# Kernel optimization log

Hardware: AMD Instinct MI355X
Metric: run time of the kernel (lower is better)

## Reference

```python
import jax, jax.numpy as jnp
import numpy as np

MOMENTUM = 0.1  # matches init_kwargs


def _amp_norm(x, running_amp, momentum):
    # x: [B, C, H, W] real; running_amp: [C, H, W]
    fft = jnp.fft.fft2(x, axes=(-2, -1))            # [B,C,H,W] complex64
    amp = jnp.abs(fft)                               # amplitude spectrum
    pha = jnp.angle(fft)                             # phase spectrum
    amp_mean = amp.mean(axis=0)                      # batch-averaged amplitude [C,H,W]
    # First call (buffer all-zero): adopt batch amplitude; otherwise EMA update.
    new_amp = jnp.where(jnp.sum(running_amp) == 0,
                        amp_mean,
                        (1.0 - momentum) * running_amp + momentum * amp_mean)
    # Rebuild spectrum with shared (running) amplitude and per-sample phase.
    fft_new = new_amp[None].astype(jnp.complex64) * jnp.exp(1j * pha)
    x_out = jnp.real(jnp.fft.ifft2(fft_new, axes=(-2, -1))).astype(x.dtype)
    return x_out, new_amp


def setup_inputs() -> dict:
    key = jax.random.key(0)
    x = jax.random.normal(key, (32, 3, 384, 384), dtype=jnp.float32)
    running_amp = jnp.zeros((3, 384, 384), dtype=jnp.float32)
    return {"x": x, "running_amp": running_amp}


def reference(x, running_amp):
    x_out, _ = _amp_norm(x, running_amp, MOMENTUM)
    return x_out
```

## Files before the change

### kernel.cpp

```cpp
#include <hip/hip_runtime.h>
#include <math.h>


#define NFFT   384
#define NL     8
#define LSTR   385
#define PADW   200
#define PLANE  147456
#define IMGS   96

__device__ __forceinline__ float2 cmul(float2 a, float2 b) {
    return make_float2(a.x*b.x - a.y*b.y, a.x*b.y + a.y*b.x);
}

__device__ __forceinline__ void fill_tw(float2* tw) {
    for (int k = threadIdx.x; k < NFFT; k += 256) {
        float ang = (-6.28318530717958647692f / (float)NFFT) * (float)k;
        float sv, cv;
        sincosf(ang, &sv, &cv);
        tw[k] = make_float2(cv, sv);
    }
}

template<int DIR>
__device__ float2* fft_lines(float2* buf0, float2* buf1, const float2* tw) {
    const int line = threadIdx.x >> 5;
    const int lane = threadIdx.x & 31;
    const float dir = (float)DIR;
    float2* src = buf0;
    float2* dst = buf1;

    {
        float2* s = src + line * LSTR;
        float2* d = dst + line * LSTR;
        const float b3 = (DIR > 0) ? -0.86602540378443864676f : 0.86602540378443864676f;
        #pragma unroll
        for (int i = 0; i < 4; ++i) {
            int j = lane + 32 * i;
            float2 c0 = s[j], c1 = s[j + 128], c2 = s[j + 256];
            float2 t0 = make_float2(c1.x + c2.x, c1.y + c2.y);
            float2 dd = make_float2(c1.x - c2.x, c1.y - c2.y);
            float2 y0 = make_float2(c0.x + t0.x, c0.y + t0.y);
            float2 u1 = make_float2(c0.x - 0.5f * t0.x, c0.y - 0.5f * t0.y);
            float2 iv = make_float2(-b3 * dd.y, b3 * dd.x);
            float2 y1 = make_float2(u1.x + iv.x, u1.y + iv.y);
            float2 y2 = make_float2(u1.x - iv.x, u1.y - iv.y);
            float2 w1 = tw[j];      w1.y *= dir;
            float2 w2 = tw[2 * j];  w2.y *= dir;
            d[3 * j]     = y0;
            d[3 * j + 1] = cmul(w1, y1);
            d[3 * j + 2] = cmul(w2, y2);
        }
    }
    __syncthreads();
    { float2* t = src; src = dst; dst = t; }

    #pragma unroll
    for (int st = 0; st < 3; ++st) {
        const int m = 3 << (2 * st);
        float2* s = src + line * LSTR;
        float2* d = dst + line * LSTR;
        #pragma unroll
        for (int i = 0; i < 3; ++i) {
            int q  = lane + 32 * i;
            int k  = q % m;
            int jm = q - k;
            float2 a = s[q], b = s[q + 96], c = s[q + 192], e = s[q + 288];
            float2 acp = make_float2(a.x + c.x, a.y + c.y);
            float2 acm = make_float2(a.x - c.x, a.y - c.y);
            float2 bdp = make_float2(b.x + e.x, b.y + e.y);
            float2 bdm = make_float2(b.x - e.x, b.y - e.y);
            float2 ibd = make_float2(-dir * bdm.y, dir * bdm.x);
            float2 y0 = make_float2(acp.x + bdp.x, acp.y + bdp.y);
            float2 y2 = make_float2(acp.x - bdp.x, acp.y - bdp.y);
            float2 y1 = make_float2(acm.x - ibd.x, acm.y - ibd.y);
            float2 y3 = make_float2(acm.x + ibd.x, acm.y + ibd.y);
            float2 w1 = tw[jm];      w1.y *= dir;
            float2 w2 = tw[2 * jm];  w2.y *= dir;
            float2 w3 = tw[3 * jm];  w3.y *= dir;
            d[4 * jm + k]         = y0;
            d[4 * jm + k + m]     = cmul(w1, y1);
            d[4 * jm + k + 2 * m] = cmul(w2, y2);
            d[4 * jm + k + 3 * m] = cmul(w3, y3);
        }
        __syncthreads();
        float2* t = src; src = dst; dst = t;
    }

    {
        float2* s = src + line * LSTR;
        float2* d = dst + line * LSTR;
        #pragma unroll
        for (int i = 0; i < 6; ++i) {
            int q = lane + 32 * i;
            float2 a = s[q];
            float2 b = s[q + 192];
            d[q]       = make_float2(a.x + b.x, a.y + b.y);
            d[q + 192] = make_float2(a.x - b.x, a.y - b.y);
        }
        __syncthreads();
        float2* t = src; src = dst; dst = t;
    }
    return src;
}

__global__ __launch_bounds__(256) void k_fft_rows_fwd(const float* __restrict__ x,
                                                      float2* __restrict__ A) {
    __shared__ float2 tw[NFFT];
    __shared__ float2 b0[NL * LSTR];
    __shared__ float2 b1[NL * LSTR];
    int bx  = blockIdx.x;
    int img = bx / 24;
    int rg  = bx - img * 24;
    fill_tw(tw);
    int line = threadIdx.x >> 5, lane = threadIdx.x & 31;
    int pr   = rg * NL + line;
    const float* xa = x + (size_t)img * PLANE + (size_t)(2 * pr) * NFFT;
    const float* xb = xa + NFFT;
    #pragma unroll
    for (int i = 0; i < 12; ++i) {
        int col = lane + 32 * i;
        b0[line * LSTR + col] = make_float2(xa[col], xb[col]);
    }
    __syncthreads();
    float2* R = fft_lines<1>(b0, b1, tw);
    float2* s = R + line * LSTR;
    float2* Aa = A + ((size_t)img * NFFT + 2 * pr) * PADW;
    float2* Ab = Aa + PADW;
    #pragma unroll
    for (int i = 0; i < 7; ++i) {
        int w = lane + 32 * i;
        if (w <= 192) {
            float2 Z  = s[w];
            float2 Zm = s[w == 0 ? 0 : NFFT - w];
            float2 Fa = make_float2(0.5f * (Z.x + Zm.x), 0.5f * (Z.y - Zm.y));
            float2 Fb = make_float2(0.5f * (Z.y + Zm.y), -0.5f * (Z.x - Zm.x));
            Aa[w] = Fa;
            Ab[w] = Fb;
        }
    }
    if (lane < 7) {
        Aa[193 + lane] = make_float2(0.0f, 0.0f);
        Ab[193 + lane] = make_float2(0.0f, 0.0f);
    }
}

__global__ __launch_bounds__(256) void k_fft_cols_fwd(float2* __restrict__ A) {
    __shared__ float2 tw[NFFT];
    __shared__ float2 b0[NL * LSTR];
    __shared__ float2 b1[NL * LSTR];
    int bx  = blockIdx.x;
    int img = bx / 25;
    int cg  = bx - img * 25;
    int w0  = cg * NL;
    fill_tw(tw);
    float2* Ai = A + (size_t)img * NFFT * PADW;
    #pragma unroll
    for (int i = 0; i < 12; ++i) {
        int idx = i * 256 + threadIdx.x;
        int h = idx >> 3, wc = idx & 7;
        b0[wc * LSTR + h] = Ai[h * PADW + w0 + wc];
    }
    __syncthreads();
    float2* R = fft_lines<1>(b0, b1, tw);
    #pragma unroll
    for (int i = 0; i < 12; ++i) {
        int idx = i * 256 + threadIdx.x;
        int h = idx >> 3, wc = idx & 7;
        Ai[h * PADW + w0 + wc] = R[wc * LSTR + h];
    }
}

__global__ __launch_bounds__(256) void k_sum_part(const float* __restrict__ r,
                                                  float* __restrict__ partial) {
    __shared__ float sm[256];
    int t = blockIdx.x * 256 + threadIdx.x;
    sm[threadIdx.x] = r[t];
    __syncthreads();
    for (int s = 128; s > 0; s >>= 1) {
        if (threadIdx.x < s) sm[threadIdx.x] += sm[threadIdx.x + s];
        __syncthreads();
    }
    if (threadIdx.x == 0) partial[blockIdx.x] = sm[0];
}

__global__ __launch_bounds__(256) void k_sum_final(const float* __restrict__ partial,
                                                   float* __restrict__ flag) {
    __shared__ float sm[256];
    float v = 0.0f;
    for (int t = threadIdx.x; t < 1728; t += 256) v += partial[t];
    sm[threadIdx.x] = v;
    __syncthreads();
    for (int s = 128; s > 0; s >>= 1) {
        if (threadIdx.x < s) sm[threadIdx.x] += sm[threadIdx.x + s];
        __syncthreads();
    }
    if (threadIdx.x == 0) flag[0] = sm[0];
}

__global__ __launch_bounds__(256) void k_amp(const float2* __restrict__ A,
                                             float* __restrict__ amp) {
    int c = blockIdx.x / NFFT;
    int h = blockIdx.x - c * NFFT;
    int w = threadIdx.x;
    if (w >= 193) return;
    float s = 0.0f;
    #pragma unroll 4
    for (int b = 0; b < 32; ++b) {
        float2 z = A[((size_t)(b * 3 + c) * NFFT + h) * PADW + w];
        s += sqrtf(z.x * z.x + z.y * z.y);
    }
    amp[((size_t)c * NFFT + h) * PADW + w] = s * (1.0f / 32.0f);
}

__global__ __launch_bounds__(256) void k_ifft_cols_scale(float2* __restrict__ A,
                                                         const float* __restrict__ ampm,
                                                         const float* __restrict__ running,
                                                         const float* __restrict__ flag) {
    __shared__ float2 tw[NFFT];
    __shared__ float2 b0[NL * LSTR];
    __shared__ float2 b1[NL * LSTR];
    int bx  = blockIdx.x;
    int img = bx / 25;
    int cg  = bx - img * 25;
    int w0  = cg * NL;
    int c   = img % 3;
    fill_tw(tw);
    bool adopt = (flag[0] == 0.0f);
    float2* Ai = A + (size_t)img * NFFT * PADW;
    #pragma unroll
    for (int i = 0; i < 12; ++i) {
        int idx = i * 256 + threadIdx.x;
        int h = idx >> 3, wc = idx & 7;
        int w = w0 + wc;
        float2 z  = Ai[h * PADW + w];
        float  am = ampm[((size_t)c * NFFT + h) * PADW + w];
        float  na;
        if (adopt) na = am;
        else {
            int wr = (w < NFFT) ? w : 0;
            na = 0.9f * running[((size_t)c * NFFT + h) * NFFT + wr] + 0.1f * am;
        }
        float mag = sqrtf(z.x * z.x + z.y * z.y);
        float2 zn;
        if (mag > 0.0f) {
            float sc = na / mag;
            zn = make_float2(z.x * sc, z.y * sc);
        } else {
            zn = make_float2(na, 0.0f);
        }
        b0[wc * LSTR + h] = zn;
    }
    __syncthreads();
    float2* R = fft_lines<-1>(b0, b1, tw);
    const float inv = 1.0f / (float)NFFT;
    #pragma unroll
    for (int i = 0; i < 12; ++i) {
        int idx = i * 256 + threadIdx.x;
        int h = idx >> 3, wc = idx & 7;
        float2 z = R[wc * LSTR + h];
        Ai[h * PADW + w0 + wc] = make_float2(z.x * inv, z.y * inv);
    }
}

__global__ __launch_bounds__(256) void k_ifft_rows_out(const float2* __restrict__ A,
                                                       float* __restrict__ out) {
    __shared__ float2 tw[NFFT];
    __shared__ float2 b0[NL * LSTR];
    __shared__ float2 b1[NL * LSTR];
    int bx  = blockIdx.x;
    int img = bx / 24;
    int rg  = bx - img * 24;
    fill_tw(tw);
    int line = threadIdx.x >> 5, lane = threadIdx.x & 31;
    int pr   = rg * NL + line;
    const float2* Aa = A + ((size_t)img * NFFT + 2 * pr) * PADW;
    const float2* Ab = Aa + PADW;
    float2* s = b0 + line * LSTR;
    #pragma unroll
    for (int i = 0; i < 7; ++i) {
        int w = lane + 32 * i;
        if (w <= 192) {
            float2 Fa = Aa[w];
            float2 Fb = Ab[w];
            s[w] = make_float2(Fa.x - Fb.y, Fa.y + Fb.x);
            if (w >= 1 && w <= 191)
                s[NFFT - w] = make_float2(Fa.x + Fb.y, Fb.x - Fa.y);
        }
    }
    __syncthreads();
    float2* R = fft_lines<-1>(b0, b1, tw);
    float2* rs = R + line * LSTR;
    const float inv = 1.0f / (float)NFFT;
    float* oa = out + (size_t)img * PLANE + (size_t)(2 * pr) * NFFT;
    float* ob = oa + NFFT;
    #pragma unroll
    for (int i = 0; i < 12; ++i) {
        int col = lane + 32 * i;
        float2 z = rs[col];
        oa[col] = z.x * inv;
        ob[col] = z.y * inv;
    }
}

extern "C" void kernel_launch(void* const* d_in, const int* in_sizes, int n_in,
                              void* d_out, int out_size, void* d_ws, size_t ws_size,
                              hipStream_t stream) {
    const float* x       = (const float*)d_in[0];
    const float* running = (const float*)d_in[1];
    float* out = (float*)d_out;

    char* ws = (char*)d_ws;
    float2* A    = (float2*)ws;
    float*  ampm = (float*)(ws + 58982400);
    float*  part = (float*)(ws + 58982400 + 921600);
    float*  flag = (float*)(ws + 58982400 + 921600 + 8192);

    k_sum_part<<<1728, 256, 0, stream>>>(running, part);
    k_sum_final<<<1, 256, 0, stream>>>(part, flag);
    k_fft_rows_fwd<<<IMGS * 24, 256, 0, stream>>>(x, A);
    k_fft_cols_fwd<<<IMGS * 25, 256, 0, stream>>>(A);
    k_amp<<<3 * NFFT, 256, 0, stream>>>(A, ampm);
    k_ifft_cols_scale<<<IMGS * 25, 256, 0, stream>>>(A, ampm, running, flag);
    k_ifft_rows_out<<<IMGS * 24, 256, 0, stream>>>(A, out);
}
```

Before: 234.3 us.

## Store intermediate spectrum in fp16 and run FFT in place with register staging

The intermediate complex spectrum buffer now holds half2 instead of float2, which halves the global traffic between the row and column FFT passes. The FFT stages load their operands into registers, sync, then write back into the same shared buffer. This drops the second ping-pong buffer and allows 5 blocks per CU through launch bounds. The amplitude kernel is flattened to one thread per element. fp16 storage of FFT coefficients (magnitudes up to a few hundred, plus small values) risks precision loss and possible overflow against the fp32 reference tolerance.

```diff
diff --git a/kernel.cpp b/kernel.cpp
--- a/kernel.cpp
+++ b/kernel.cpp
@@ -1,4 +1,5 @@
 #include <hip/hip_runtime.h>
+#include <hip/hip_fp16.h>
 #include <math.h>
 
 
@@ -6,6 +7,7 @@
 #define NL     8
 #define LSTR   385
 #define PADW   200
+#define HPLANE (NFFT * PADW)
 #define PLANE  147456
 #define IMGS   96
 
@@ -23,21 +25,24 @@
 }
 
 template<int DIR>
-__device__ float2* fft_lines(float2* buf0, float2* buf1, const float2* tw) {
-    const int line = threadIdx.x >> 5;
-    const int lane = threadIdx.x & 31;
+__device__ void fft_sb(float2* s, const float2* tw, int lane) {
     const float dir = (float)DIR;
-    float2* src = buf0;
-    float2* dst = buf1;
-
+    float2 r[12];
+
+    #pragma unroll
+    for (int i = 0; i < 4; ++i) {
+        int j = lane + 32 * i;
+        r[3*i]   = s[j];
+        r[3*i+1] = s[j + 128];
+        r[3*i+2] = s[j + 256];
+    }
+    __syncthreads();
     {
-        float2* s = src + line * LSTR;
-        float2* d = dst + line * LSTR;
         const float b3 = (DIR > 0) ? -0.86602540378443864676f : 0.86602540378443864676f;
         #pragma unroll
         for (int i = 0; i < 4; ++i) {
             int j = lane + 32 * i;
-            float2 c0 = s[j], c1 = s[j + 128], c2 = s[j + 256];
+            float2 c0 = r[3*i], c1 = r[3*i+1], c2 = r[3*i+2];
             float2 t0 = make_float2(c1.x + c2.x, c1.y + c2.y);
             float2 dd = make_float2(c1.x - c2.x, c1.y - c2.y);
             float2 y0 = make_float2(c0.x + t0.x, c0.y + t0.y);
@@ -47,25 +52,31 @@
             float2 y2 = make_float2(u1.x - iv.x, u1.y - iv.y);
             float2 w1 = tw[j];      w1.y *= dir;
             float2 w2 = tw[2 * j];  w2.y *= dir;
-            d[3 * j]     = y0;
-            d[3 * j + 1] = cmul(w1, y1);
-            d[3 * j + 2] = cmul(w2, y2);
-        }
-    }
-    __syncthreads();
-    { float2* t = src; src = dst; dst = t; }
+            s[3 * j]     = y0;
+            s[3 * j + 1] = cmul(w1, y1);
+            s[3 * j + 2] = cmul(w2, y2);
+        }
+    }
+    __syncthreads();
 
     #pragma unroll
     for (int st = 0; st < 3; ++st) {
         const int m = 3 << (2 * st);
-        float2* s = src + line * LSTR;
-        float2* d = dst + line * LSTR;
+        #pragma unroll
+        for (int i = 0; i < 3; ++i) {
+            int q = lane + 32 * i;
+            r[4*i]   = s[q];
+            r[4*i+1] = s[q + 96];
+            r[4*i+2] = s[q + 192];
+            r[4*i+3] = s[q + 288];
+        }
+        __syncthreads();
         #pragma unroll
         for (int i = 0; i < 3; ++i) {
             int q  = lane + 32 * i;
             int k  = q % m;
             int jm = q - k;
-            float2 a = s[q], b = s[q + 96], c = s[q + 192], e = s[q + 288];
+            float2 a = r[4*i], b = r[4*i+1], c = r[4*i+2], e = r[4*i+3];
             float2 acp = make_float2(a.x + c.x, a.y + c.y);
             float2 acm = make_float2(a.x - c.x, a.y - c.y);
             float2 bdp = make_float2(b.x + e.x, b.y + e.y);
@@ -78,37 +89,29 @@
             float2 w1 = tw[jm];      w1.y *= dir;
             float2 w2 = tw[2 * jm];  w2.y *= dir;
             float2 w3 = tw[3 * jm];  w3.y *= dir;
-            d[4 * jm + k]         = y0;
-            d[4 * jm + k + m]     = cmul(w1, y1);
-            d[4 * jm + k + 2 * m] = cmul(w2, y2);
-            d[4 * jm + k + 3 * m] = cmul(w3, y3);
+            s[4 * jm + k]         = y0;
+            s[4 * jm + k + m]     = cmul(w1, y1);
+            s[4 * jm + k + 2 * m] = cmul(w2, y2);
+            s[4 * jm + k + 3 * m] = cmul(w3, y3);
         }
         __syncthreads();
-        float2* t = src; src = dst; dst = t;
-    }
-
-    {
-        float2* s = src + line * LSTR;
-        float2* d = dst + line * LSTR;
-        #pragma unroll
-        for (int i = 0; i < 6; ++i) {
-            int q = lane + 32 * i;
-            float2 a = s[q];
-            float2 b = s[q + 192];
-            d[q]       = make_float2(a.x + b.x, a.y + b.y);
-            d[q + 192] = make_float2(a.x - b.x, a.y - b.y);
-        }
-        __syncthreads();
-        float2* t = src; src = dst; dst = t;
-    }
-    return src;
-}
-
-__global__ __launch_bounds__(256) void k_fft_rows_fwd(const float* __restrict__ x,
-                                                      float2* __restrict__ A) {
+    }
+
+    #pragma unroll
+    for (int i = 0; i < 6; ++i) {
+        int q = lane + 32 * i;
+        float2 a = s[q];
+        float2 b = s[q + 192];
+        s[q]       = make_float2(a.x + b.x, a.y + b.y);
+        s[q + 192] = make_float2(a.x - b.x, a.y - b.y);
+    }
+    __syncthreads();
+}
+
+__global__ __launch_bounds__(256, 5) void k_fft_rows_fwd(const float* __restrict__ x,
+                                                         __half2* __restrict__ A) {
     __shared__ float2 tw[NFFT];
     __shared__ float2 b0[NL * LSTR];
-    __shared__ float2 b1[NL * LSTR];
     int bx  = blockIdx.x;
     int img = bx / 24;
     int rg  = bx - img * 24;
@@ -117,57 +120,56 @@
     int pr   = rg * NL + line;
     const float* xa = x + (size_t)img * PLANE + (size_t)(2 * pr) * NFFT;
     const float* xb = xa + NFFT;
+    float2* s = b0 + line * LSTR;
     #pragma unroll
     for (int i = 0; i < 12; ++i) {
         int col = lane + 32 * i;
-        b0[line * LSTR + col] = make_float2(xa[col], xb[col]);
-    }
-    __syncthreads();
-    float2* R = fft_lines<1>(b0, b1, tw);
-    float2* s = R + line * LSTR;
-    float2* Aa = A + ((size_t)img * NFFT + 2 * pr) * PADW;
-    float2* Ab = Aa + PADW;
+        s[col] = make_float2(xa[col], xb[col]);
+    }
+    __syncthreads();
+    fft_sb<1>(s, tw, lane);
+    __half2* Aa = A + ((size_t)img * NFFT + 2 * pr) * PADW;
+    __half2* Ab = Aa + PADW;
     #pragma unroll
     for (int i = 0; i < 7; ++i) {
         int w = lane + 32 * i;
         if (w <= 192) {
             float2 Z  = s[w];
             float2 Zm = s[w == 0 ? 0 : NFFT - w];
-            float2 Fa = make_float2(0.5f * (Z.x + Zm.x), 0.5f * (Z.y - Zm.y));
-            float2 Fb = make_float2(0.5f * (Z.y + Zm.y), -0.5f * (Z.x - Zm.x));
-            Aa[w] = Fa;
-            Ab[w] = Fb;
+            Aa[w] = __floats2half2_rn(0.5f * (Z.x + Zm.x),  0.5f * (Z.y - Zm.y));
+            Ab[w] = __floats2half2_rn(0.5f * (Z.y + Zm.y), -0.5f * (Z.x - Zm.x));
         }
     }
     if (lane < 7) {
-        Aa[193 + lane] = make_float2(0.0f, 0.0f);
-        Ab[193 + lane] = make_float2(0.0f, 0.0f);
-    }
-}
-
-__global__ __launch_bounds__(256) void k_fft_cols_fwd(float2* __restrict__ A) {
+        Aa[193 + lane] = __floats2half2_rn(0.0f, 0.0f);
+        Ab[193 + lane] = __floats2half2_rn(0.0f, 0.0f);
+    }
+}
+
+__global__ __launch_bounds__(256, 5) void k_fft_cols_fwd(__half2* __restrict__ A) {
     __shared__ float2 tw[NFFT];
     __shared__ float2 b0[NL * LSTR];
-    __shared__ float2 b1[NL * LSTR];
     int bx  = blockIdx.x;
     int img = bx / 25;
     int cg  = bx - img * 25;
     int w0  = cg * NL;
     fill_tw(tw);
-    float2* Ai = A + (size_t)img * NFFT * PADW;
+    __half2* Ai = A + (size_t)img * HPLANE;
     #pragma unroll
     for (int i = 0; i < 12; ++i) {
         int idx = i * 256 + threadIdx.x;
         int h = idx >> 3, wc = idx & 7;
-        b0[wc * LSTR + h] = Ai[h * PADW + w0 + wc];
-    }
-    __syncthreads();
-    float2* R = fft_lines<1>(b0, b1, tw);
+        b0[wc * LSTR + h] = __half22float2(Ai[h * PADW + w0 + wc]);
+    }
+    __syncthreads();
+    int line = threadIdx.x >> 5, lane = threadIdx.x & 31;
+    fft_sb<1>(b0 + line * LSTR, tw, lane);
     #pragma unroll
     for (int i = 0; i < 12; ++i) {
         int idx = i * 256 + threadIdx.x;
         int h = idx >> 3, wc = idx & 7;
-        Ai[h * PADW + w0 + wc] = R[wc * LSTR + h];
+        float2 z = b0[wc * LSTR + h];
+        Ai[h * PADW + w0 + wc] = __floats2half2_rn(z.x, z.y);
     }
 }
 
@@ -198,28 +200,26 @@
     if (threadIdx.x == 0) flag[0] = sm[0];
 }
 
-__global__ __launch_bounds__(256) void k_amp(const float2* __restrict__ A,
+__global__ __launch_bounds__(256) void k_amp(const __half2* __restrict__ A,
                                              float* __restrict__ amp) {
-    int c = blockIdx.x / NFFT;
-    int h = blockIdx.x - c * NFFT;
-    int w = threadIdx.x;
-    if (w >= 193) return;
+    int t = blockIdx.x * 256 + threadIdx.x;
+    int c  = t / HPLANE;
+    int hw = t - c * HPLANE;
     float s = 0.0f;
     #pragma unroll 4
     for (int b = 0; b < 32; ++b) {
-        float2 z = A[((size_t)(b * 3 + c) * NFFT + h) * PADW + w];
+        float2 z = __half22float2(A[(size_t)(b * 3 + c) * HPLANE + hw]);
         s += sqrtf(z.x * z.x + z.y * z.y);
     }
-    amp[((size_t)c * NFFT + h) * PADW + w] = s * (1.0f / 32.0f);
-}
-
-__global__ __launch_bounds__(256) void k_ifft_cols_scale(float2* __restrict__ A,
-                                                         const float* __restrict__ ampm,
-                                                         const float* __restrict__ running,
-                                                         const float* __restrict__ flag) {
+    amp[t] = s * (1.0f / 32.0f);
+}
+
+__global__ __launch_bounds__(256, 5) void k_ifft_cols_scale(__half2* __restrict__ A,
+                                                            const float* __restrict__ ampm,
+                                                            const float* __restrict__ running,
+                                                            const float* __restrict__ flag) {
     __shared__ float2 tw[NFFT];
     __shared__ float2 b0[NL * LSTR];
-    __shared__ float2 b1[NL * LSTR];
     int bx  = blockIdx.x;
     int img = bx / 25;
     int cg  = bx - img * 25;
@@ -227,14 +227,14 @@
     int c   = img % 3;
     fill_tw(tw);
     bool adopt = (flag[0] == 0.0f);
-    float2* Ai = A + (size_t)img * NFFT * PADW;
+    __half2* Ai = A + (size_t)img * HPLANE;
     #pragma unroll
     for (int i = 0; i < 12; ++i) {
         int idx = i * 256 + threadIdx.x;
         int h = idx >> 3, wc = idx & 7;
         int w = w0 + wc;
-        float2 z  = Ai[h * PADW + w];
-        float  am = ampm[((size_t)c * NFFT + h) * PADW + w];
+        float2 z  = __half22float2(Ai[h * PADW + w]);
+        float  am = ampm[(size_t)c * HPLANE + h * PADW + w];
         float  na;
         if (adopt) na = am;
         else {
@@ -252,52 +252,51 @@
         b0[wc * LSTR + h] = zn;
     }
     __syncthreads();
-    float2* R = fft_lines<-1>(b0, b1, tw);
+    int line = threadIdx.x >> 5, lane = threadIdx.x & 31;
+    fft_sb<-1>(b0 + line * LSTR, tw, lane);
     const float inv = 1.0f / (float)NFFT;
     #pragma unroll
     for (int i = 0; i < 12; ++i) {
         int idx = i * 256 + threadIdx.x;
         int h = idx >> 3, wc = idx & 7;
-        float2 z = R[wc * LSTR + h];
-        Ai[h * PADW + w0 + wc] = make_float2(z.x * inv, z.y * inv);
-    }
-}
-
-__global__ __launch_bounds__(256) void k_ifft_rows_out(const float2* __restrict__ A,
-                                                       float* __restrict__ out) {
+        float2 z = b0[wc * LSTR + h];
+        Ai[h * PADW + w0 + wc] = __floats2half2_rn(z.x * inv, z.y * inv);
+    }
+}
+
+__global__ __launch_bounds__(256, 5) void k_ifft_rows_out(const __half2* __restrict__ A,
+                                                          float* __restrict__ out) {
     __shared__ float2 tw[NFFT];
     __shared__ float2 b0[NL * LSTR];
-    __shared__ float2 b1[NL * LSTR];
     int bx  = blockIdx.x;
     int img = bx / 24;
     int rg  = bx - img * 24;
     fill_tw(tw);
     int line = threadIdx.x >> 5, lane = threadIdx.x & 31;
     int pr   = rg * NL + line;
-    const float2* Aa = A + ((size_t)img * NFFT + 2 * pr) * PADW;
-    const float2* Ab = Aa + PADW;
+    const __half2* Aa = A + ((size_t)img * NFFT + 2 * pr) * PADW;
+    const __half2* Ab = Aa + PADW;
     float2* s = b0 + line * LSTR;
     #pragma unroll
     for (int i = 0; i < 7; ++i) {
         int w = lane + 32 * i;
         if (w <= 192) {
-            float2 Fa = Aa[w];
-            float2 Fb = Ab[w];
+            float2 Fa = __half22float2(Aa[w]);
+            float2 Fb = __half22float2(Ab[w]);
             s[w] = make_float2(Fa.x - Fb.y, Fa.y + Fb.x);
             if (w >= 1 && w <= 191)
                 s[NFFT - w] = make_float2(Fa.x + Fb.y, Fb.x - Fa.y);
         }
     }
     __syncthreads();
-    float2* R = fft_lines<-1>(b0, b1, tw);
-    float2* rs = R + line * LSTR;
+    fft_sb<-1>(s, tw, lane);
     const float inv = 1.0f / (float)NFFT;
     float* oa = out + (size_t)img * PLANE + (size_t)(2 * pr) * NFFT;
     float* ob = oa + NFFT;
     #pragma unroll
     for (int i = 0; i < 12; ++i) {
         int col = lane + 32 * i;
-        float2 z = rs[col];
+        float2 z = s[col];
         oa[col] = z.x * inv;
         ob[col] = z.y * inv;
     }
@@ -311,16 +310,16 @@
     float* out = (float*)d_out;
 
     char* ws = (char*)d_ws;
-    float2* A    = (float2*)ws;
-    float*  ampm = (float*)(ws + 58982400);
-    float*  part = (float*)(ws + 58982400 + 921600);
-    float*  flag = (float*)(ws + 58982400 + 921600 + 8192);
+    __half2* A    = (__half2*)ws;
+    float*   ampm = (float*)(ws + 29491200);
+    float*   part = (float*)(ws + 29491200 + 921600);
+    float*   flag = (float*)(ws + 29491200 + 921600 + 8192);
 
     k_sum_part<<<1728, 256, 0, stream>>>(running, part);
     k_sum_final<<<1, 256, 0, stream>>>(part, flag);
     k_fft_rows_fwd<<<IMGS * 24, 256, 0, stream>>>(x, A);
     k_fft_cols_fwd<<<IMGS * 25, 256, 0, stream>>>(A);
-    k_amp<<<3 * NFFT, 256, 0, stream>>>(A, ampm);
+    k_amp<<<(3 * HPLANE) / 256, 256, 0, stream>>>(A, ampm);
     k_ifft_cols_scale<<<IMGS * 25, 256, 0, stream>>>(A, ampm, running, flag);
     k_ifft_rows_out<<<IMGS * 24, 256, 0, stream>>>(A, out);
 }
```

Result: slower. 277.3 us (+18.3%).
